# Kernel optimization log

Measured on AMD Instinct MI355X. Metric: run time of the kernel, lower is better.

## Reference

```python
import jax, jax.numpy as jnp
import numpy as np

FP8_MAX = 448.0   # float8_e4m3fn max finite value (target_dtype='e4m3')
PARAM1 = 1.0      # scale margin multiplier (config.param1)
PARAM2 = 1e-12    # amax epsilon floor (config.param2)


def setup_inputs() -> dict:
    key = jax.random.key(0)
    x = jax.random.normal(key, (8192, 8192), dtype=jnp.float32)
    return {"x": x}


def reference(x) -> jnp.ndarray:
    # per-channel granularity: one scale per last-dim channel, amax over all
    # leading dims. shape of amax: [1, ..., C]
    reduce_axes = tuple(range(x.ndim - 1))
    amax = jnp.max(jnp.abs(x), axis=reduce_axes, keepdims=True)
    scale = (FP8_MAX * PARAM1) / jnp.maximum(amax, PARAM2)   # [1, C]
    # scale, round-to-nearest via real e4m3 cast (saturating clamp first), dequant
    xs = jnp.clip(x * scale, -FP8_MAX, FP8_MAX)
    q = xs.astype(jnp.float8_e4m3fn).astype(x.dtype)
    return q / scale
```

## Files before the change

kernel.cpp:

```cpp
#include <hip/hip_runtime.h>
#include <stdint.h>

#define N_COLS 8192
#define N_ROWS 8192
#define FP8_MAX_F 448.0f
#define EPS_F 1e-12f

static __device__ __forceinline__ float fakequant(float x, float s) {
    float xs = x * s;
    xs = fminf(fmaxf(xs, -FP8_MAX_F), FP8_MAX_F);
    int p = __builtin_amdgcn_cvt_pk_fp8_f32(xs, xs, 0, false);
    float q = __builtin_amdgcn_cvt_f32_fp8(p, 0);
    return q / s;
}

__global__ __launch_bounds__(256) void zero_ws_kernel(uint32_t* __restrict__ amax) {
    int i = blockIdx.x * 256 + threadIdx.x;
    if (i < N_COLS) amax[i] = 0u;
}

__global__ __launch_bounds__(256) void col_amax_kernel(const float4* __restrict__ x4,
                                                       uint32_t* __restrict__ amax,
                                                       int rows_per_block) {
    const int C4 = N_COLS / 4;
    int c4 = blockIdx.x * 256 + threadIdx.x;
    int r0 = blockIdx.y * rows_per_block;
    uint32_t m0 = 0, m1 = 0, m2 = 0, m3 = 0;
    const float4* p = x4 + (size_t)r0 * C4 + c4;
    for (int r = 0; r < rows_per_block; ++r) {
        float4 v = p[(size_t)r * C4];
        m0 = max(m0, __float_as_uint(v.x) & 0x7FFFFFFFu);
        m1 = max(m1, __float_as_uint(v.y) & 0x7FFFFFFFu);
        m2 = max(m2, __float_as_uint(v.z) & 0x7FFFFFFFu);
        m3 = max(m3, __float_as_uint(v.w) & 0x7FFFFFFFu);
    }
    int c = c4 * 4;
    atomicMax((unsigned int*)&amax[c + 0], m0);
    atomicMax((unsigned int*)&amax[c + 1], m1);
    atomicMax((unsigned int*)&amax[c + 2], m2);
    atomicMax((unsigned int*)&amax[c + 3], m3);
}

__global__ __launch_bounds__(256) void scale_kernel(const uint32_t* __restrict__ amax,
                                                    float* __restrict__ scale) {
    int c = blockIdx.x * 256 + threadIdx.x;
    if (c < N_COLS) {
        float a = __uint_as_float(amax[c]);
        a = fmaxf(a, EPS_F);
        scale[c] = FP8_MAX_F / a;
    }
}

__global__ __launch_bounds__(256) void quant_kernel(const float4* __restrict__ x4,
                                                    const float4* __restrict__ scale4,
                                                    float4* __restrict__ out4,
                                                    size_t n4) {
    const int C4 = N_COLS / 4;
    size_t stride = (size_t)gridDim.x * 256;
    for (size_t i = (size_t)blockIdx.x * 256 + threadIdx.x; i < n4; i += stride) {
        float4 s = scale4[i & (size_t)(C4 - 1)];
        float4 v = x4[i];
        float4 o;
        o.x = fakequant(v.x, s.x);
        o.y = fakequant(v.y, s.y);
        o.z = fakequant(v.z, s.z);
        o.w = fakequant(v.w, s.w);
        out4[i] = o;
    }
}

extern "C" void kernel_launch(void* const* d_in, const int* in_sizes, int n_in,
                              void* d_out, int out_size, void* d_ws, size_t ws_size,
                              hipStream_t stream) {
    const float* x = (const float*)d_in[0];
    float* out = (float*)d_out;
    uint32_t* amax = (uint32_t*)d_ws;
    float* scale = (float*)((char*)d_ws + N_COLS * sizeof(uint32_t));

    zero_ws_kernel<<<N_COLS / 256, 256, 0, stream>>>(amax);

    const int ROWCHUNKS = 128;
    dim3 g1(N_COLS / 1024, ROWCHUNKS);
    col_amax_kernel<<<g1, 256, 0, stream>>>((const float4*)x, amax,
                                            N_ROWS / ROWCHUNKS);

    scale_kernel<<<N_COLS / 256, 256, 0, stream>>>(amax, scale);

    size_t n4 = (size_t)N_ROWS * N_COLS / 4;
    quant_kernel<<<2048, 256, 0, stream>>>((const float4*)x, (const float4*)scale,
                                           (float4*)out, n4);
}
```

Baseline: 167.3 us.

## Replace atomic amax with partial reductions, precompute inverse scale, nontemporal stores

Column amax is written as per-chunk partial maxima and reduced in a second kernel, removing the workspace zeroing launch and the global atomics. The scale kernel also stores the reciprocal so the quant kernel multiplies instead of dividing. The quant kernel packs four fp8 conversions and uses nontemporal stores for the output. The reciprocal multiply may differ slightly in rounding from the reference division, and the workspace grows to hold the partials.

```diff
diff --git a/kernel.cpp b/kernel.cpp
--- a/kernel.cpp
+++ b/kernel.cpp
@@ -3,69 +3,71 @@
 
 #define N_COLS 8192
 #define N_ROWS 8192
+#define C4 (N_COLS / 4)
 #define FP8_MAX_F 448.0f
 #define EPS_F 1e-12f
+#define ROWCHUNKS 128
+#define ROWS_PER_BLOCK (N_ROWS / ROWCHUNKS)
 
-static __device__ __forceinline__ float fakequant(float x, float s) {
-    float xs = x * s;
-    xs = fminf(fmaxf(xs, -FP8_MAX_F), FP8_MAX_F);
-    int p = __builtin_amdgcn_cvt_pk_fp8_f32(xs, xs, 0, false);
-    float q = __builtin_amdgcn_cvt_f32_fp8(p, 0);
-    return q / s;
-}
+typedef float floatx4 __attribute__((ext_vector_type(4)));
 
-__global__ __launch_bounds__(256) void zero_ws_kernel(uint32_t* __restrict__ amax) {
-    int i = blockIdx.x * 256 + threadIdx.x;
-    if (i < N_COLS) amax[i] = 0u;
-}
-
-__global__ __launch_bounds__(256) void col_amax_kernel(const float4* __restrict__ x4,
-                                                       uint32_t* __restrict__ amax,
-                                                       int rows_per_block) {
-    const int C4 = N_COLS / 4;
+__global__ __launch_bounds__(256) void col_amax_partial(const float4* __restrict__ x4,
+                                                        float4* __restrict__ partial4) {
     int c4 = blockIdx.x * 256 + threadIdx.x;
-    int r0 = blockIdx.y * rows_per_block;
+    const float4* p = x4 + (size_t)blockIdx.y * ROWS_PER_BLOCK * C4 + c4;
     uint32_t m0 = 0, m1 = 0, m2 = 0, m3 = 0;
-    const float4* p = x4 + (size_t)r0 * C4 + c4;
-    for (int r = 0; r < rows_per_block; ++r) {
+#pragma unroll 8
+    for (int r = 0; r < ROWS_PER_BLOCK; ++r) {
         float4 v = p[(size_t)r * C4];
         m0 = max(m0, __float_as_uint(v.x) & 0x7FFFFFFFu);
         m1 = max(m1, __float_as_uint(v.y) & 0x7FFFFFFFu);
         m2 = max(m2, __float_as_uint(v.z) & 0x7FFFFFFFu);
         m3 = max(m3, __float_as_uint(v.w) & 0x7FFFFFFFu);
     }
-    int c = c4 * 4;
-    atomicMax((unsigned int*)&amax[c + 0], m0);
-    atomicMax((unsigned int*)&amax[c + 1], m1);
-    atomicMax((unsigned int*)&amax[c + 2], m2);
-    atomicMax((unsigned int*)&amax[c + 3], m3);
+    float4 o;
+    o.x = __uint_as_float(m0);
+    o.y = __uint_as_float(m1);
+    o.z = __uint_as_float(m2);
+    o.w = __uint_as_float(m3);
+    partial4[(size_t)blockIdx.y * C4 + c4] = o;
 }
 
-__global__ __launch_bounds__(256) void scale_kernel(const uint32_t* __restrict__ amax,
-                                                    float* __restrict__ scale) {
+__global__ __launch_bounds__(256) void scale_from_partials(const float* __restrict__ partial,
+                                                           float* __restrict__ scale,
+                                                           float* __restrict__ inv) {
     int c = blockIdx.x * 256 + threadIdx.x;
-    if (c < N_COLS) {
-        float a = __uint_as_float(amax[c]);
-        a = fmaxf(a, EPS_F);
-        scale[c] = FP8_MAX_F / a;
-    }
+    float a = 0.0f;
+#pragma unroll 8
+    for (int k = 0; k < ROWCHUNKS; ++k)
+        a = fmaxf(a, partial[(size_t)k * N_COLS + c]);
+    a = fmaxf(a, EPS_F);
+    scale[c] = FP8_MAX_F / a;
+    inv[c]   = a / FP8_MAX_F;
 }
 
 __global__ __launch_bounds__(256) void quant_kernel(const float4* __restrict__ x4,
                                                     const float4* __restrict__ scale4,
-                                                    float4* __restrict__ out4,
-                                                    size_t n4) {
-    const int C4 = N_COLS / 4;
+                                                    const float4* __restrict__ inv4,
+                                                    floatx4* __restrict__ out4) {
+    const size_t n4 = (size_t)N_ROWS * C4;
     size_t stride = (size_t)gridDim.x * 256;
     for (size_t i = (size_t)blockIdx.x * 256 + threadIdx.x; i < n4; i += stride) {
-        float4 s = scale4[i & (size_t)(C4 - 1)];
+        size_t ci = i & (size_t)(C4 - 1);
+        float4 s = scale4[ci];
+        float4 w = inv4[ci];
         float4 v = x4[i];
-        float4 o;
-        o.x = fakequant(v.x, s.x);
-        o.y = fakequant(v.y, s.y);
-        o.z = fakequant(v.z, s.z);
-        o.w = fakequant(v.w, s.w);
-        out4[i] = o;
+        float a0 = fminf(fmaxf(v.x * s.x, -FP8_MAX_F), FP8_MAX_F);
+        float a1 = fminf(fmaxf(v.y * s.y, -FP8_MAX_F), FP8_MAX_F);
+        float a2 = fminf(fmaxf(v.z * s.z, -FP8_MAX_F), FP8_MAX_F);
+        float a3 = fminf(fmaxf(v.w * s.w, -FP8_MAX_F), FP8_MAX_F);
+        int p = __builtin_amdgcn_cvt_pk_fp8_f32(a0, a1, 0, false);
+        p = __builtin_amdgcn_cvt_pk_fp8_f32(a2, a3, p, true);
+        floatx4 o;
+        o.x = __builtin_amdgcn_cvt_f32_fp8(p, 0) * w.x;
+        o.y = __builtin_amdgcn_cvt_f32_fp8(p, 1) * w.y;
+        o.z = __builtin_amdgcn_cvt_f32_fp8(p, 2) * w.z;
+        o.w = __builtin_amdgcn_cvt_f32_fp8(p, 3) * w.w;
+        __builtin_nontemporal_store(o, &out4[i]);
     }
 }
 
@@ -74,19 +76,15 @@
                               hipStream_t stream) {
     const float* x = (const float*)d_in[0];
     float* out = (float*)d_out;
-    uint32_t* amax = (uint32_t*)d_ws;
-    float* scale = (float*)((char*)d_ws + N_COLS * sizeof(uint32_t));
+    float* partial = (float*)d_ws;
+    float* scale = (float*)((char*)d_ws + (size_t)ROWCHUNKS * N_COLS * sizeof(float));
+    float* inv = scale + N_COLS;
 
-    zero_ws_kernel<<<N_COLS / 256, 256, 0, stream>>>(amax);
+    dim3 g1(N_COLS / 1024, ROWCHUNKS);
+    col_amax_partial<<<g1, 256, 0, stream>>>((const float4*)x, (float4*)partial);
 
-    const int ROWCHUNKS = 128;
-    dim3 g1(N_COLS / 1024, ROWCHUNKS);
-    col_amax_kernel<<<g1, 256, 0, stream>>>((const float4*)x, amax,
-                                            N_ROWS / ROWCHUNKS);
+    scale_from_partials<<<N_COLS / 256, 256, 0, stream>>>(partial, scale, inv);
 
-    scale_kernel<<<N_COLS / 256, 256, 0, stream>>>(amax, scale);
-
-    size_t n4 = (size_t)N_ROWS * N_COLS / 4;
     quant_kernel<<<2048, 256, 0, stream>>>((const float4*)x, (const float4*)scale,
-                                           (float4*)out, n4);
+                                           (const float4*)inv, (floatx4*)out);
 }
```

Result: faster. 150.8 us (-9.9%).
